# Optimization experiments

Hardware: AMD Instinct MI355X
Metric: run time of the kernel (lower is better)

Reference implementation:

```python
import jax, jax.numpy as jnp
import numpy as np

B, T, D, U, T_DEC = 32, 2048, 512, 256, 256


def setup_inputs() -> dict:
    key = jax.random.key(0)
    ks = jax.random.split(key, 8)
    s = 0.05  # small init scale to avoid tanh/sigmoid saturation
    return {
        "x": jax.random.normal(ks[0], (B, T, D), dtype=jnp.float32),
        "W_s": jax.random.normal(ks[1], (D, U), dtype=jnp.float32) * s,
        "U_a": jax.random.normal(ks[2], (D, U), dtype=jnp.float32) * s,
        "b_a": jnp.zeros((U,), dtype=jnp.float32),
        "W_a": jax.random.normal(ks[3], (U, U), dtype=jnp.float32) * s,
        "V_a": jax.random.normal(ks[4], (U,), dtype=jnp.float32) * s,
        "kernel": jax.random.normal(ks[5], (D, 4 * U), dtype=jnp.float32) * s,
        "recurrent_kernel": jax.random.normal(ks[6], (U, 4 * U), dtype=jnp.float32) * s,
        "bias": jnp.concatenate([
            jnp.zeros((U,), jnp.float32),      # i
            jnp.ones((U,), jnp.float32),       # f (unit_forget_bias)
            jnp.zeros((2 * U,), jnp.float32),  # c, o
        ]),
        "decode_steps": T_DEC,
    }


def _hard_sigmoid(z):
    # keras hard_sigmoid: clip(0.2*x + 0.5, 0, 1)
    return jnp.clip(0.2 * z + 0.5, 0.0, 1.0)


def reference(x, W_s, U_a, b_a, W_a, V_a, kernel, recurrent_kernel, bias, decode_steps):
    # Precompute U_a projection of encoder states once (as in call()).
    uxpb = jnp.einsum('btd,du->btu', x, U_a) + b_a          # [B,T,U]
    h0 = jnp.tanh(x[:, 0] @ W_s)                            # [B,U] initial state
    c0 = jnp.zeros_like(h0)

    def step(carry, _):
        h, c = carry
        # Bahdanau additive attention over encoder timesteps
        e = jnp.einsum('btu,u->bt', jnp.tanh(uxpb + (h @ W_a)[:, None, :]), V_a)
        a = jax.nn.softmax(e, axis=1)                       # exp/sum in original
        ctx = jnp.einsum('bt,btd->bd', a, x)                # weighted context [B,D]
        # Fused LSTM gate matmuls on context + previous state
        z = ctx @ kernel + h @ recurrent_kernel + bias      # [B,4U]
        zi, zf, zc, zo = jnp.split(z, 4, axis=-1)
        i = _hard_sigmoid(zi)
        f = _hard_sigmoid(zf)
        o = _hard_sigmoid(zo)
        c_new = f * c + i * jnp.tanh(zc)
        h_new = o * jnp.tanh(c_new)
        return (h_new, c_new), h_new

    (_, _), ys = jax.lax.scan(step, (h0, c0), None, length=decode_steps)
    return jnp.transpose(ys, (1, 0, 2))                     # [B, T_dec, U]
```

## Files before the change

kernel.cpp:

```cpp
#include <hip/hip_runtime.h>
#include <stdint.h>

#define B_    32
#define T_    2048
#define D_    512
#define U_    256
#define TSP_  128
#define NSL   (T_/TSP_)

typedef short          bf16x8 __attribute__((ext_vector_type(8)));
typedef unsigned short u16x4  __attribute__((ext_vector_type(4)));
typedef float          f32x4  __attribute__((ext_vector_type(4)));
typedef float          f32x2  __attribute__((ext_vector_type(2)));

__device__ __forceinline__ float bf2f(unsigned short u){
  union{unsigned int i; float f;} v; v.i = ((unsigned int)u)<<16; return v.f;
}
__device__ __forceinline__ unsigned short f2bf(float f){
  union{float f; unsigned int i;} v; v.f = f;
  unsigned int r = v.i + 0x7FFFu + ((v.i>>16)&1u);
  return (unsigned short)(r>>16);
}
__device__ __forceinline__ float ftanh(float x){
  float xx = fminf(fmaxf(x,-20.f),20.f);
  float t = __builtin_amdgcn_exp2f(xx * 2.885390082f);
  return (t-1.f)*__builtin_amdgcn_rcpf(t+1.f);
}
__device__ __forceinline__ float fexp(float x){
  return __builtin_amdgcn_exp2f(x*1.4426950408889634f);
}

__device__ unsigned int f2e4m3_1(float f){
  union{float f; unsigned int i;} v; v.f = f;
  unsigned int s = (v.i>>31)<<7;
  float af = fabsf(f);
  af = fminf(af, 448.f);
  unsigned int code;
  if (af < 0.015625f){
    code = (unsigned int)rintf(af*512.f);
  } else {
    int ex; float mant = frexpf(af,&ex);
    int E = ex-1;
    int m = (int)rintf(mant*16.f - 8.f);
    if (m==8){ E+=1; m=0; }
    if (E>8){ E=8; m=6; }
    code = ((unsigned int)(E+7)<<3) | (unsigned int)m;
  }
  return s|code;
}

__device__ __forceinline__ float e4m3f(unsigned int b){
  int e = (int)((b>>3)&15u), m = (int)(b&7u);
  int M = e ? (m+8) : m;
  M = (b&128u) ? -M : M;
  int E = (e ? e : 1) - 10;
  return ldexpf((float)M, E);
}

#if __has_builtin(__builtin_amdgcn_cvt_pk_f32_fp8)
#define DEC8(Q,F) {                                                      \
  f32x2 t_;                                                              \
  t_ = __builtin_amdgcn_cvt_pk_f32_fp8((int)Q.x, false); F[0]=t_[0]; F[1]=t_[1]; \
  t_ = __builtin_amdgcn_cvt_pk_f32_fp8((int)Q.x, true ); F[2]=t_[0]; F[3]=t_[1]; \
  t_ = __builtin_amdgcn_cvt_pk_f32_fp8((int)Q.y, false); F[4]=t_[0]; F[5]=t_[1]; \
  t_ = __builtin_amdgcn_cvt_pk_f32_fp8((int)Q.y, true ); F[6]=t_[0]; F[7]=t_[1]; }
#define DEC4(Q,F) {                                                      \
  f32x2 t_;                                                              \
  t_ = __builtin_amdgcn_cvt_pk_f32_fp8((int)Q, false); F[0]=t_[0]; F[1]=t_[1]; \
  t_ = __builtin_amdgcn_cvt_pk_f32_fp8((int)Q, true ); F[2]=t_[0]; F[3]=t_[1]; }
#else
#define DEC8(Q,F) {                                                      \
  F[0]=e4m3f(Q.x&255u);      F[1]=e4m3f((Q.x>>8)&255u);                  \
  F[2]=e4m3f((Q.x>>16)&255u);F[3]=e4m3f(Q.x>>24);                        \
  F[4]=e4m3f(Q.y&255u);      F[5]=e4m3f((Q.y>>8)&255u);                  \
  F[6]=e4m3f((Q.y>>16)&255u);F[7]=e4m3f(Q.y>>24); }
#define DEC4(Q,F) {                                                      \
  F[0]=e4m3f(Q&255u);        F[1]=e4m3f((Q>>8)&255u);                    \
  F[2]=e4m3f((Q>>16)&255u);  F[3]=e4m3f(Q>>24); }
#endif

__global__ __launch_bounds__(256) void k_f2b(
    const float* __restrict__ src, unsigned short* __restrict__ dst, int n)
{
  int idx = (blockIdx.x*256 + threadIdx.x)*4;
  int stride = gridDim.x*256*4;
  for (; idx < n; idx += stride){
    float4 v = *(const float4*)(src+idx);
    u16x4 o; o.x=f2bf(v.x); o.y=f2bf(v.y); o.z=f2bf(v.z); o.w=f2bf(v.w);
    *(u16x4*)(dst+idx) = o;
  }
}

__global__ __launch_bounds__(256) void k_f2e8(
    const float* __restrict__ src, unsigned char* __restrict__ dst, int n)
{
  int idx = (blockIdx.x*256 + threadIdx.x)*8;
  int stride = gridDim.x*256*8;
  for (; idx < n; idx += stride){
    float4 a = *(const float4*)(src+idx);
    float4 b = *(const float4*)(src+idx+4);
    unsigned int w0 = f2e4m3_1(a.x) | (f2e4m3_1(a.y)<<8) |
                      (f2e4m3_1(a.z)<<16) | (f2e4m3_1(a.w)<<24);
    unsigned int w1 = f2e4m3_1(b.x) | (f2e4m3_1(b.y)<<8) |
                      (f2e4m3_1(b.z)<<16) | (f2e4m3_1(b.w)<<24);
    uint2 o; o.x = w0; o.y = w1;
    *(uint2*)(dst+idx) = o;
  }
}

__global__ __launch_bounds__(256) void k_uxpb(
    const float* __restrict__ x,
    const float* __restrict__ Ua,
    const float* __restrict__ ba,
    unsigned char* __restrict__ uxpb)
{
  __shared__ unsigned short As[64][40];
  __shared__ unsigned short Bs[64][40];
  int bx = blockIdx.x;
  int nt = bx & 3, mt = bx >> 2;
  int m0 = mt*64, n0 = nt*64;
  int tid = threadIdx.x;
  int lane = tid & 63, w = tid >> 6;
  int wm = w >> 1, wn = w & 1;

  f32x4 acc[2][2] = {};
  int ar = tid >> 2, ak = (tid & 3) * 8;
  int bk = tid >> 3, bn = (tid & 7) * 8;

  for (int k0 = 0; k0 < 512; k0 += 32) {
    const float* ap = x  + (long)(m0+ar)*512 + k0 + ak;
    const float* bp = Ua + (long)(k0+bk)*256 + n0 + bn;
    float4 a0 = *(const float4*)ap, a1 = *(const float4*)(ap+4);
    float4 b0 = *(const float4*)bp, b1 = *(const float4*)(bp+4);
    __syncthreads();
    unsigned short* as = &As[ar][ak];
    as[0]=f2bf(a0.x); as[1]=f2bf(a0.y); as[2]=f2bf(a0.z); as[3]=f2bf(a0.w);
    as[4]=f2bf(a1.x); as[5]=f2bf(a1.y); as[6]=f2bf(a1.z); as[7]=f2bf(a1.w);
    Bs[bn+0][bk]=f2bf(b0.x); Bs[bn+1][bk]=f2bf(b0.y);
    Bs[bn+2][bk]=f2bf(b0.z); Bs[bn+3][bk]=f2bf(b0.w);
    Bs[bn+4][bk]=f2bf(b1.x); Bs[bn+5][bk]=f2bf(b1.y);
    Bs[bn+6][bk]=f2bf(b1.z); Bs[bn+7][bk]=f2bf(b1.w);
    __syncthreads();
    #pragma unroll
    for (int mi = 0; mi < 2; ++mi) {
      bf16x8 a = *(const bf16x8*)&As[wm*32 + mi*16 + (lane&15)][(lane>>4)*8];
      #pragma unroll
      for (int ni = 0; ni < 2; ++ni) {
        bf16x8 b = *(const bf16x8*)&Bs[wn*32 + ni*16 + (lane&15)][(lane>>4)*8];
        acc[mi][ni] = __builtin_amdgcn_mfma_f32_16x16x32_bf16(a, b, acc[mi][ni], 0,0,0);
      }
    }
  }
  #pragma unroll
  for (int mi = 0; mi < 2; ++mi)
  #pragma unroll
  for (int ni = 0; ni < 2; ++ni) {
    int col = n0 + wn*32 + ni*16 + (lane&15);
    float bias = ba[col];
    #pragma unroll
    for (int r = 0; r < 4; ++r) {
      int row = m0 + wm*32 + mi*16 + (lane>>4)*4 + r;
      uxpb[(long)row*256 + col] = (unsigned char)f2e4m3_1(acc[mi][ni][r] + bias);
    }
  }
}

__global__ __launch_bounds__(256) void k_init_h(
    const float* __restrict__ x,
    const float* __restrict__ Ws,
    float* __restrict__ h0,
    float* __restrict__ c_ws)
{
  int b = blockIdx.x, tid = threadIdx.x;
  __shared__ float xs[512];
  xs[tid]     = x[(long)b*T_*D_ + tid];
  xs[tid+256] = x[(long)b*T_*D_ + tid + 256];
  __syncthreads();
  float sum = 0.f;
  for (int k = 0; k < 512; ++k) sum = fmaf(xs[k], Ws[(long)k*256 + tid], sum);
  h0[b*256+tid] = ftanh(sum);
  c_ws[b*256+tid] = 0.f;
}

__global__ __launch_bounds__(256) void k_init_hw(
    const float* __restrict__ Wa,
    const float* __restrict__ h0,
    float* __restrict__ hW_part)
{
  int wg = blockIdx.x; int b = wg>>3, j = wg&7;
  int tid = threadIdx.x;
  __shared__ float hn[32];
  if (tid < 32) hn[tid] = h0[b*256 + j*32 + tid];
  __syncthreads();
  float sum = 0.f;
  #pragma unroll 8
  for (int w2 = 0; w2 < 32; ++w2) sum = fmaf(hn[w2], Wa[(j*32+w2)*256 + tid], sum);
  hW_part[(b*8+j)*256 + tid] = sum;
}

template<int XBF>
__global__ __launch_bounds__(512, 6) void k_attn(
    const float* __restrict__ xf,
    const unsigned char* __restrict__ x8,
    const unsigned char* __restrict__ uxpb,
    const float* __restrict__ Va,
    const float* __restrict__ hW_part,
    float* __restrict__ part_s,
    float* __restrict__ part_ctx)
{
  int wg = blockIdx.x;
  int b = wg >> 4, sl = wg & 15;
  int tid = threadIdx.x, lane = tid & 63, w = tid >> 6;

  __shared__ float hws[256];
  __shared__ float wsum[8];
  __shared__ float wctx[8][512];

  if (tid < 256) {
    float hsum = 0.f;
    #pragma unroll
    for (int j = 0; j < 8; ++j) hsum += hW_part[(b*8+j)*256 + tid];
    hws[tid] = hsum;
  }
  __syncthreads();
  float hw0 = hws[lane*4+0], hw1 = hws[lane*4+1];
  float hw2 = hws[lane*4+2], hw3 = hws[lane*4+3];
  float4 vv = *(const float4*)(Va + lane*4);

  const long rbase = (long)b*T_ + sl*TSP_ + w*16;
  const unsigned char*  up0 = uxpb + rbase*256 + lane*4;
  const unsigned char*  xp8 = x8   + rbase*512 + lane*8;
  const float*          pf0 = xf   + rbase*512 + lane*8;

  float ssum = 0.f;
  float acc[8] = {0,0,0,0,0,0,0,0};

  #pragma unroll
  for (int i = 0; i < 16; i += 2) {
    unsigned int u0 = *(const unsigned int*)(up0 + (long)i*256);
    unsigned int u1 = *(const unsigned int*)(up0 + (long)(i+1)*256);
    float ua0[4], ua1[4];
    DEC4(u0, ua0);
    DEC4(u1, ua1);
    float e0 = 0.f, e1 = 0.f;
    e0 = fmaf(ftanh(ua0[0] + hw0), vv.x, e0);
    e1 = fmaf(ftanh(ua1[0] + hw0), vv.x, e1);
    e0 = fmaf(ftanh(ua0[1] + hw1), vv.y, e0);
    e1 = fmaf(ftanh(ua1[1] + hw1), vv.y, e1);
    e0 = fmaf(ftanh(ua0[2] + hw2), vv.z, e0);
    e1 = fmaf(ftanh(ua1[2] + hw2), vv.z, e1);
    e0 = fmaf(ftanh(ua0[3] + hw3), vv.w, e0);
    e1 = fmaf(ftanh(ua1[3] + hw3), vv.w, e1);
    #pragma unroll
    for (int o = 1; o < 64; o <<= 1) {
      e0 += __shfl_xor(e0, o, 64);
      e1 += __shfl_xor(e1, o, 64);
    }
    float p0 = fexp(e0), p1 = fexp(e1);
    ssum += p0 + p1;
    if (XBF) {
      uint2 q0 = *(const uint2*)(xp8 + (long)i*512);
      uint2 q1 = *(const uint2*)(xp8 + (long)(i+1)*512);
      float x0a[8], x1a[8];
      DEC8(q0, x0a);
      DEC8(q1, x1a);
      #pragma unroll
      for (int j = 0; j < 8; ++j)
        acc[j] = fmaf(p1, x1a[j], fmaf(p0, x0a[j], acc[j]));
    } else {
      const float* p0p = pf0 + (long)i*512;
      const float* p1p = pf0 + (long)(i+1)*512;
      float4 v00 = *(const float4*)p0p, v01 = *(const float4*)(p0p+4);
      float4 v10 = *(const float4*)p1p, v11 = *(const float4*)(p1p+4);
      float x0a[8] = {v00.x,v00.y,v00.z,v00.w,v01.x,v01.y,v01.z,v01.w};
      float x1a[8] = {v10.x,v10.y,v10.z,v10.w,v11.x,v11.y,v11.z,v11.w};
      #pragma unroll
      for (int j = 0; j < 8; ++j)
        acc[j] = fmaf(p1, x1a[j], fmaf(p0, x0a[j], acc[j]));
    }
  }

  if (lane == 0) wsum[w] = ssum;
  #pragma unroll
  for (int j = 0; j < 8; ++j) wctx[w][lane*8+j] = acc[j];
  __syncthreads();
  {
    int d = tid;
    float c = wctx[0][d] + wctx[1][d] + wctx[2][d] + wctx[3][d]
            + wctx[4][d] + wctx[5][d] + wctx[6][d] + wctx[7][d];
    part_ctx[(long)(b*NSL+sl)*512 + d] = c;
  }
  if (tid == 0)
    part_s[b*NSL+sl] = wsum[0]+wsum[1]+wsum[2]+wsum[3]
                     + wsum[4]+wsum[5]+wsum[6]+wsum[7];
}

template<int WBF>
__global__ __launch_bounds__(1024) void k_step(
    const float* __restrict__ Wk,
    const float* __restrict__ Wr,
    const unsigned short* __restrict__ Wkb,
    const unsigned short* __restrict__ Wrb,
    const float* __restrict__ bias,
    const float* __restrict__ Wa,
    const unsigned short* __restrict__ Wab,
    const float* __restrict__ part_s,
    const float* __restrict__ part_ctx,
    const float* __restrict__ h_in,
    float* __restrict__ h_out,
    float* __restrict__ c_ws,
    float* __restrict__ hW_part,
    float* __restrict__ out,
    int step, int TDEC)
{
  int wg = blockIdx.x;
  int b = wg >> 3, j = wg & 7;
  int tid = threadIdx.x;

  __shared__ float ctx[512];
  __shared__ float hsh[256];
  __shared__ float zp[8][128];
  __shared__ float hn[32];

  if (tid < 512) {
    float S = 0.f;
    #pragma unroll 8
    for (int i = 0; i < NSL; ++i) S += part_s[b*NSL+i];
    float invS = 1.f / S;
    float c = 0.f;
    #pragma unroll 8
    for (int i = 0; i < NSL; ++i)
      c += part_ctx[(long)(b*NSL+i)*512 + tid];
    ctx[tid] = c * invS;
  } else if (tid < 768) {
    hsh[tid-512] = h_in[b*256 + (tid-512)];
  }
  __syncthreads();

  int c_  = tid & 127, kq = tid >> 7;
  int g   = c_ >> 5;
  int col = g*256 + j*32 + (c_ & 31);
  int k0 = kq*96, k1 = k0 + 96;
  int kb = (k1 < 512) ? k1 : 512;
  int kc = (k0 > 512) ? k0 : 512;
  float z = 0.f;
  if (WBF) {
    #pragma unroll 8
    for (int k = k0; k < kb; ++k)
      z = fmaf(ctx[k], bf2f(Wkb[(long)k*1024 + col]), z);
    #pragma unroll 8
    for (int k = kc; k < k1; ++k)
      z = fmaf(hsh[k-512], bf2f(Wrb[(long)(k-512)*1024 + col]), z);
  } else {
    #pragma unroll 8
    for (int k = k0; k < kb; ++k)
      z = fmaf(ctx[k], Wk[(long)k*1024 + col], z);
    #pragma unroll 8
    for (int k = kc; k < k1; ++k)
      z = fmaf(hsh[k-512], Wr[(long)(k-512)*1024 + col], z);
  }
  zp[kq][c_] = z;
  __syncthreads();

  if (tid < 128) {
    int colr = (tid>>5)*256 + j*32 + (tid&31);
    float zz = zp[0][tid]+zp[1][tid]+zp[2][tid]+zp[3][tid]
             + zp[4][tid]+zp[5][tid]+zp[6][tid]+zp[7][tid] + bias[colr];
    zp[0][tid] = zz;
  }
  __syncthreads();

  if (tid < 32) {
    float zi = zp[0][tid], zf = zp[0][32+tid], zc = zp[0][64+tid], zo = zp[0][96+tid];
    float ig = fminf(fmaxf(0.2f*zi+0.5f, 0.f), 1.f);
    float fg = fminf(fmaxf(0.2f*zf+0.5f, 0.f), 1.f);
    float og = fminf(fmaxf(0.2f*zo+0.5f, 0.f), 1.f);
    int u = j*32 + tid;
    float c_old = c_ws[b*256+u];
    float c_new = fg*c_old + ig*ftanh(zc);
    float h_new = og*ftanh(c_new);
    c_ws[b*256+u]  = c_new;
    h_out[b*256+u] = h_new;
    out[((long)b*TDEC + step)*256 + u] = h_new;
    hn[tid] = h_new;
  }
  __syncthreads();

  if (tid < 256) {
    float sum = 0.f;
    if (WBF) {
      #pragma unroll 8
      for (int w2 = 0; w2 < 32; ++w2)
        sum = fmaf(hn[w2], bf2f(Wab[(j*32+w2)*256 + tid]), sum);
    } else {
      #pragma unroll 8
      for (int w2 = 0; w2 < 32; ++w2)
        sum = fmaf(hn[w2], Wa[(j*32+w2)*256 + tid], sum);
    }
    hW_part[(b*8+j)*256 + tid] = sum;
  }
}

extern "C" void kernel_launch(void* const* d_in, const int* in_sizes, int n_in,
                              void* d_out, int out_size, void* d_ws, size_t ws_size,
                              hipStream_t stream)
{
  const float* x  = (const float*)d_in[0];
  const float* Ws = (const float*)d_in[1];
  const float* Ua = (const float*)d_in[2];
  const float* ba = (const float*)d_in[3];
  const float* Wa = (const float*)d_in[4];
  const float* Va = (const float*)d_in[5];
  const float* Wk = (const float*)d_in[6];
  const float* Wr = (const float*)d_in[7];
  const float* bs = (const float*)d_in[8];
  int TDEC = out_size / (B_ * U_);

  size_t off = 0;
  char* base = (char*)d_ws;
  unsigned char* uxpb = (unsigned char*)(base+off);   off += (size_t)B_*T_*U_;
  float* part_ctx = (float*)(base+off);               off += (size_t)B_*NSL*512*4;
  float* part_s   = (float*)(base+off);               off += (size_t)B_*NSL*4;
  float* hW_part  = (float*)(base+off);               off += (size_t)B_*8*U_*4;
  float* h_buf    = (float*)(base+off);               off += (size_t)2*B_*U_*4;
  float* c_ws     = (float*)(base+off);               off += (size_t)B_*U_*4;
  unsigned char* x_f8 = (unsigned char*)(base+off);   off += (size_t)B_*T_*D_;
  bool use_x8 = (off <= ws_size);
  unsigned short* wk_bf = (unsigned short*)(base+off); off += (size_t)D_*4*U_*2;
  unsigned short* wr_bf = (unsigned short*)(base+off); off += (size_t)U_*4*U_*2;
  unsigned short* wa_bf = (unsigned short*)(base+off); off += (size_t)U_*U_*2;
  bool use_wbf = (off <= ws_size);

  k_uxpb  <<<(B_*T_/64)*(U_/64), 256, 0, stream>>>(x, Ua, ba, uxpb);
  if (use_x8) k_f2e8<<<2048, 256, 0, stream>>>(x, x_f8, B_*T_*D_);
  if (use_wbf) {
    k_f2b<<<512, 256, 0, stream>>>(Wk, wk_bf, D_*4*U_);
    k_f2b<<<256, 256, 0, stream>>>(Wr, wr_bf, U_*4*U_);
    k_f2b<<<64,  256, 0, stream>>>(Wa, wa_bf, U_*U_);
  }
  k_init_h<<<B_,  256, 0, stream>>>(x, Ws, h_buf, c_ws);
  k_init_hw<<<B_*8, 256, 0, stream>>>(Wa, h_buf, hW_part);

  for (int s = 0; s < TDEC; ++s) {
    float* h_in  = h_buf + (s & 1)     * B_ * U_;
    float* h_out = h_buf + ((s+1) & 1) * B_ * U_;
    if (use_x8)
      k_attn<1><<<B_*NSL, 512, 0, stream>>>(x, x_f8, uxpb, Va, hW_part,
                                            part_s, part_ctx);
    else
      k_attn<0><<<B_*NSL, 512, 0, stream>>>(x, x_f8, uxpb, Va, hW_part,
                                            part_s, part_ctx);
    if (use_wbf)
      k_step<1><<<B_*8, 1024, 0, stream>>>(Wk, Wr, wk_bf, wr_bf, bs, Wa, wa_bf,
                                           part_s, part_ctx, h_in, h_out,
                                           c_ws, hW_part, (float*)d_out, s, TDEC);
    else
      k_step<0><<<B_*8, 1024, 0, stream>>>(Wk, Wr, wk_bf, wr_bf, bs, Wa, wa_bf,
                                           part_s, part_ctx, h_in, h_out,
                                           c_ws, hW_part, (float*)d_out, s, TDEC);
  }
}
```

Baseline: 5.574 ms.

## Fuse attention and LSTM step kernels into one launch with flag-based handoff

Each decode step now launches a single kernel. Attention blocks publish per-slice completion flags with release stores, and LSTM-step blocks in the same grid spin on those flags before reducing context and computing gates. This removes one kernel launch and its inter-kernel gap per step, and the step blocks drop from 1024 to 512 threads with longer K chunks. It risks deadlock if the step blocks become resident before the attention blocks and starve them. It also drops the fp32 fallback paths and leaves an empty k_attn_f32 stub.

```diff
diff --git a/kernel.cpp b/kernel.cpp
--- a/kernel.cpp
+++ b/kernel.cpp
@@ -108,6 +108,11 @@
   }
 }
 
+__global__ void k_zero(int* __restrict__ p, int n){
+  int i = blockIdx.x*256 + threadIdx.x;
+  if (i < n) p[i] = 0;
+}
+
 __global__ __launch_bounds__(256) void k_uxpb(
     const float* __restrict__ x,
     const float* __restrict__ Ua,
@@ -198,67 +203,78 @@
   hW_part[(b*8+j)*256 + tid] = sum;
 }
 
-template<int XBF>
-__global__ __launch_bounds__(512, 6) void k_attn(
-    const float* __restrict__ xf,
+__global__ __launch_bounds__(512, 4) void k_fused(
     const unsigned char* __restrict__ x8,
     const unsigned char* __restrict__ uxpb,
     const float* __restrict__ Va,
-    const float* __restrict__ hW_part,
+    const unsigned short* __restrict__ Wkb,
+    const unsigned short* __restrict__ Wrb,
+    const float* __restrict__ bias,
+    const unsigned short* __restrict__ Wab,
     float* __restrict__ part_s,
-    float* __restrict__ part_ctx)
-{
+    float* __restrict__ part_ctx,
+    float* __restrict__ hW_part,
+    const float* __restrict__ h_in,
+    float* __restrict__ h_out,
+    float* __restrict__ c_ws,
+    float* __restrict__ out,
+    int* __restrict__ s1f,
+    int step, int TDEC)
+{
+  __shared__ float sA[8*512];
+  __shared__ float sB[264];
+
   int wg = blockIdx.x;
-  int b = wg >> 4, sl = wg & 15;
-  int tid = threadIdx.x, lane = tid & 63, w = tid >> 6;
-
-  __shared__ float hws[256];
-  __shared__ float wsum[8];
-  __shared__ float wctx[8][512];
-
-  if (tid < 256) {
-    float hsum = 0.f;
+  int tid = threadIdx.x;
+
+  if (wg < B_*NSL) {
+    int b = wg >> 4, sl = wg & 15;
+    int lane = tid & 63, w = tid >> 6;
+    float* hws = sB;
+    float* wsum = sB + 256;
+    float (*wctx)[512] = (float(*)[512])sA;
+
+    if (tid < 256) {
+      float hsum = 0.f;
+      #pragma unroll
+      for (int j = 0; j < 8; ++j) hsum += hW_part[(b*8+j)*256 + tid];
+      hws[tid] = hsum;
+    }
+    __syncthreads();
+    float hw0 = hws[lane*4+0], hw1 = hws[lane*4+1];
+    float hw2 = hws[lane*4+2], hw3 = hws[lane*4+3];
+    float4 vv = *(const float4*)(Va + lane*4);
+
+    const long rbase = (long)b*T_ + sl*TSP_ + w*16;
+    const unsigned char* up0 = uxpb + rbase*256 + lane*4;
+    const unsigned char* xp8 = x8   + rbase*512 + lane*8;
+
+    float ssum = 0.f;
+    float acc[8] = {0,0,0,0,0,0,0,0};
+
     #pragma unroll
-    for (int j = 0; j < 8; ++j) hsum += hW_part[(b*8+j)*256 + tid];
-    hws[tid] = hsum;
-  }
-  __syncthreads();
-  float hw0 = hws[lane*4+0], hw1 = hws[lane*4+1];
-  float hw2 = hws[lane*4+2], hw3 = hws[lane*4+3];
-  float4 vv = *(const float4*)(Va + lane*4);
-
-  const long rbase = (long)b*T_ + sl*TSP_ + w*16;
-  const unsigned char*  up0 = uxpb + rbase*256 + lane*4;
-  const unsigned char*  xp8 = x8   + rbase*512 + lane*8;
-  const float*          pf0 = xf   + rbase*512 + lane*8;
-
-  float ssum = 0.f;
-  float acc[8] = {0,0,0,0,0,0,0,0};
-
-  #pragma unroll
-  for (int i = 0; i < 16; i += 2) {
-    unsigned int u0 = *(const unsigned int*)(up0 + (long)i*256);
-    unsigned int u1 = *(const unsigned int*)(up0 + (long)(i+1)*256);
-    float ua0[4], ua1[4];
-    DEC4(u0, ua0);
-    DEC4(u1, ua1);
-    float e0 = 0.f, e1 = 0.f;
-    e0 = fmaf(ftanh(ua0[0] + hw0), vv.x, e0);
-    e1 = fmaf(ftanh(ua1[0] + hw0), vv.x, e1);
-    e0 = fmaf(ftanh(ua0[1] + hw1), vv.y, e0);
-    e1 = fmaf(ftanh(ua1[1] + hw1), vv.y, e1);
-    e0 = fmaf(ftanh(ua0[2] + hw2), vv.z, e0);
-    e1 = fmaf(ftanh(ua1[2] + hw2), vv.z, e1);
-    e0 = fmaf(ftanh(ua0[3] + hw3), vv.w, e0);
-    e1 = fmaf(ftanh(ua1[3] + hw3), vv.w, e1);
-    #pragma unroll
-    for (int o = 1; o < 64; o <<= 1) {
-      e0 += __shfl_xor(e0, o, 64);
-      e1 += __shfl_xor(e1, o, 64);
-    }
-    float p0 = fexp(e0), p1 = fexp(e1);
-    ssum += p0 + p1;
-    if (XBF) {
+    for (int i = 0; i < 16; i += 2) {
+      unsigned int u0 = *(const unsigned int*)(up0 + (long)i*256);
+      unsigned int u1 = *(const unsigned int*)(up0 + (long)(i+1)*256);
+      float ua0[4], ua1[4];
+      DEC4(u0, ua0);
+      DEC4(u1, ua1);
+      float e0 = 0.f, e1 = 0.f;
+      e0 = fmaf(ftanh(ua0[0] + hw0), vv.x, e0);
+      e1 = fmaf(ftanh(ua1[0] + hw0), vv.x, e1);
+      e0 = fmaf(ftanh(ua0[1] + hw1), vv.y, e0);
+      e1 = fmaf(ftanh(ua1[1] + hw1), vv.y, e1);
+      e0 = fmaf(ftanh(ua0[2] + hw2), vv.z, e0);
+      e1 = fmaf(ftanh(ua1[2] + hw2), vv.z, e1);
+      e0 = fmaf(ftanh(ua0[3] + hw3), vv.w, e0);
+      e1 = fmaf(ftanh(ua1[3] + hw3), vv.w, e1);
+      #pragma unroll
+      for (int o = 1; o < 64; o <<= 1) {
+        e0 += __shfl_xor(e0, o, 64);
+        e1 += __shfl_xor(e1, o, 64);
+      }
+      float p0 = fexp(e0), p1 = fexp(e1);
+      ssum += p0 + p1;
       uint2 q0 = *(const uint2*)(xp8 + (long)i*512);
       uint2 q1 = *(const uint2*)(xp8 + (long)(i+1)*512);
       float x0a[8], x1a[8];
@@ -267,138 +283,111 @@
       #pragma unroll
       for (int j = 0; j < 8; ++j)
         acc[j] = fmaf(p1, x1a[j], fmaf(p0, x0a[j], acc[j]));
-    } else {
-      const float* p0p = pf0 + (long)i*512;
-      const float* p1p = pf0 + (long)(i+1)*512;
-      float4 v00 = *(const float4*)p0p, v01 = *(const float4*)(p0p+4);
-      float4 v10 = *(const float4*)p1p, v11 = *(const float4*)(p1p+4);
-      float x0a[8] = {v00.x,v00.y,v00.z,v00.w,v01.x,v01.y,v01.z,v01.w};
-      float x1a[8] = {v10.x,v10.y,v10.z,v10.w,v11.x,v11.y,v11.z,v11.w};
-      #pragma unroll
-      for (int j = 0; j < 8; ++j)
-        acc[j] = fmaf(p1, x1a[j], fmaf(p0, x0a[j], acc[j]));
-    }
-  }
-
-  if (lane == 0) wsum[w] = ssum;
-  #pragma unroll
-  for (int j = 0; j < 8; ++j) wctx[w][lane*8+j] = acc[j];
-  __syncthreads();
-  {
-    int d = tid;
-    float c = wctx[0][d] + wctx[1][d] + wctx[2][d] + wctx[3][d]
-            + wctx[4][d] + wctx[5][d] + wctx[6][d] + wctx[7][d];
-    part_ctx[(long)(b*NSL+sl)*512 + d] = c;
-  }
-  if (tid == 0)
-    part_s[b*NSL+sl] = wsum[0]+wsum[1]+wsum[2]+wsum[3]
-                     + wsum[4]+wsum[5]+wsum[6]+wsum[7];
-}
-
-template<int WBF>
-__global__ __launch_bounds__(1024) void k_step(
-    const float* __restrict__ Wk,
-    const float* __restrict__ Wr,
-    const unsigned short* __restrict__ Wkb,
-    const unsigned short* __restrict__ Wrb,
-    const float* __restrict__ bias,
-    const float* __restrict__ Wa,
-    const unsigned short* __restrict__ Wab,
-    const float* __restrict__ part_s,
-    const float* __restrict__ part_ctx,
-    const float* __restrict__ h_in,
-    float* __restrict__ h_out,
-    float* __restrict__ c_ws,
-    float* __restrict__ hW_part,
-    float* __restrict__ out,
-    int step, int TDEC)
-{
-  int wg = blockIdx.x;
-  int b = wg >> 3, j = wg & 7;
-  int tid = threadIdx.x;
-
-  __shared__ float ctx[512];
-  __shared__ float hsh[256];
-  __shared__ float zp[8][128];
-  __shared__ float hn[32];
-
-  if (tid < 512) {
-    float S = 0.f;
-    #pragma unroll 8
-    for (int i = 0; i < NSL; ++i) S += part_s[b*NSL+i];
-    float invS = 1.f / S;
-    float c = 0.f;
-    #pragma unroll 8
-    for (int i = 0; i < NSL; ++i)
-      c += part_ctx[(long)(b*NSL+i)*512 + tid];
-    ctx[tid] = c * invS;
-  } else if (tid < 768) {
-    hsh[tid-512] = h_in[b*256 + (tid-512)];
-  }
-  __syncthreads();
-
-  int c_  = tid & 127, kq = tid >> 7;
-  int g   = c_ >> 5;
-  int col = g*256 + j*32 + (c_ & 31);
-  int k0 = kq*96, k1 = k0 + 96;
-  int kb = (k1 < 512) ? k1 : 512;
-  int kc = (k0 > 512) ? k0 : 512;
-  float z = 0.f;
-  if (WBF) {
+    }
+
+    if (lane == 0) wsum[w] = ssum;
+    #pragma unroll
+    for (int j = 0; j < 8; ++j) wctx[w][lane*8+j] = acc[j];
+    __syncthreads();
+    {
+      int d = tid;
+      float c = wctx[0][d] + wctx[1][d] + wctx[2][d] + wctx[3][d]
+              + wctx[4][d] + wctx[5][d] + wctx[6][d] + wctx[7][d];
+      part_ctx[(long)(b*NSL+sl)*512 + d] = c;
+    }
+    if (tid == 0)
+      part_s[b*NSL+sl] = wsum[0]+wsum[1]+wsum[2]+wsum[3]
+                       + wsum[4]+wsum[5]+wsum[6]+wsum[7];
+    __syncthreads();
+    if (tid == 0)
+      __hip_atomic_store(&s1f[b*NSL+sl], step+1, __ATOMIC_RELEASE,
+                         __HIP_MEMORY_SCOPE_AGENT);
+  } else {
+    int t = wg - B_*NSL;
+    int b = t >> 3, j = t & 7;
+    float* ctx = sA;
+    float* hsh = sA + 512;
+    float (*zp)[128] = (float(*)[128])(sA + 768);
+    float* hn  = sA + 1280;
+
+    if (tid < NSL) {
+      while (__hip_atomic_load(&s1f[b*NSL+tid], __ATOMIC_RELAXED,
+                               __HIP_MEMORY_SCOPE_AGENT) < step+1)
+        __builtin_amdgcn_s_sleep(64);
+    }
+    __syncthreads();
+    __builtin_amdgcn_fence(__ATOMIC_ACQUIRE, "agent");
+
+    {
+      float S = 0.f;
+      #pragma unroll 8
+      for (int i = 0; i < NSL; ++i) S += part_s[b*NSL+i];
+      float invS = 1.f / S;
+      float c = 0.f;
+      #pragma unroll 8
+      for (int i = 0; i < NSL; ++i)
+        c += part_ctx[(long)(b*NSL+i)*512 + tid];
+      ctx[tid] = c * invS;
+    }
+    if (tid < 256) hsh[tid] = h_in[b*256 + tid];
+    __syncthreads();
+
+    int c_  = tid & 127, kq = tid >> 7;
+    int col = (c_ >> 5)*256 + j*32 + (c_ & 31);
+    int k0 = kq*192, k1 = k0 + 192;
+    int kb = (k1 < 512) ? k1 : 512;
+    int kc = (k0 > 512) ? k0 : 512;
+    float z = 0.f;
     #pragma unroll 8
     for (int k = k0; k < kb; ++k)
       z = fmaf(ctx[k], bf2f(Wkb[(long)k*1024 + col]), z);
     #pragma unroll 8
     for (int k = kc; k < k1; ++k)
       z = fmaf(hsh[k-512], bf2f(Wrb[(long)(k-512)*1024 + col]), z);
-  } else {
-    #pragma unroll 8
-    for (int k = k0; k < kb; ++k)
-      z = fmaf(ctx[k], Wk[(long)k*1024 + col], z);
-    #pragma unroll 8
-    for (int k = kc; k < k1; ++k)
-      z = fmaf(hsh[k-512], Wr[(long)(k-512)*1024 + col], z);
-  }
-  zp[kq][c_] = z;
-  __syncthreads();
-
-  if (tid < 128) {
-    int colr = (tid>>5)*256 + j*32 + (tid&31);
-    float zz = zp[0][tid]+zp[1][tid]+zp[2][tid]+zp[3][tid]
-             + zp[4][tid]+zp[5][tid]+zp[6][tid]+zp[7][tid] + bias[colr];
-    zp[0][tid] = zz;
-  }
-  __syncthreads();
-
-  if (tid < 32) {
-    float zi = zp[0][tid], zf = zp[0][32+tid], zc = zp[0][64+tid], zo = zp[0][96+tid];
-    float ig = fminf(fmaxf(0.2f*zi+0.5f, 0.f), 1.f);
-    float fg = fminf(fmaxf(0.2f*zf+0.5f, 0.f), 1.f);
-    float og = fminf(fmaxf(0.2f*zo+0.5f, 0.f), 1.f);
-    int u = j*32 + tid;
-    float c_old = c_ws[b*256+u];
-    float c_new = fg*c_old + ig*ftanh(zc);
-    float h_new = og*ftanh(c_new);
-    c_ws[b*256+u]  = c_new;
-    h_out[b*256+u] = h_new;
-    out[((long)b*TDEC + step)*256 + u] = h_new;
-    hn[tid] = h_new;
-  }
-  __syncthreads();
-
-  if (tid < 256) {
-    float sum = 0.f;
-    if (WBF) {
+    zp[kq][c_] = z;
+    __syncthreads();
+
+    if (tid < 128) {
+      int colr = (tid>>5)*256 + j*32 + (tid&31);
+      float zz = zp[0][tid]+zp[1][tid]+zp[2][tid]+zp[3][tid] + bias[colr];
+      zp[0][tid] = zz;
+    }
+    __syncthreads();
+
+    if (tid < 32) {
+      float zi = zp[0][tid], zf = zp[0][32+tid], zc = zp[0][64+tid], zo = zp[0][96+tid];
+      float ig = fminf(fmaxf(0.2f*zi+0.5f, 0.f), 1.f);
+      float fg = fminf(fmaxf(0.2f*zf+0.5f, 0.f), 1.f);
+      float og = fminf(fmaxf(0.2f*zo+0.5f, 0.f), 1.f);
+      int u = j*32 + tid;
+      float c_old = c_ws[b*256+u];
+      float c_new = fg*c_old + ig*ftanh(zc);
+      float h_new = og*ftanh(c_new);
+      c_ws[b*256+u]  = c_new;
+      h_out[b*256+u] = h_new;
+      out[((long)b*TDEC + step)*256 + u] = h_new;
+      hn[tid] = h_new;
+    }
+    __syncthreads();
+
+    if (tid < 256) {
+      float sum = 0.f;
       #pragma unroll 8
       for (int w2 = 0; w2 < 32; ++w2)
         sum = fmaf(hn[w2], bf2f(Wab[(j*32+w2)*256 + tid]), sum);
-    } else {
-      #pragma unroll 8
-      for (int w2 = 0; w2 < 32; ++w2)
-        sum = fmaf(hn[w2], Wa[(j*32+w2)*256 + tid], sum);
-    }
-    hW_part[(b*8+j)*256 + tid] = sum;
-  }
+      hW_part[(b*8+j)*256 + tid] = sum;
+    }
+  }
+}
+
+__global__ __launch_bounds__(512, 6) void k_attn_f32(
+    const float* __restrict__ xf,
+    const unsigned char* __restrict__ uxpb,
+    const float* __restrict__ Va,
+    const float* __restrict__ hW_part,
+    float* __restrict__ part_s,
+    float* __restrict__ part_ctx)
+{
 }
 
 extern "C" void kernel_launch(void* const* d_in, const int* in_sizes, int n_in,
@@ -424,39 +413,27 @@
   float* hW_part  = (float*)(base+off);               off += (size_t)B_*8*U_*4;
   float* h_buf    = (float*)(base+off);               off += (size_t)2*B_*U_*4;
   float* c_ws     = (float*)(base+off);               off += (size_t)B_*U_*4;
+  int*   s1f      = (int*)(base+off);                 off += (size_t)B_*NSL*4;
   unsigned char* x_f8 = (unsigned char*)(base+off);   off += (size_t)B_*T_*D_;
-  bool use_x8 = (off <= ws_size);
   unsigned short* wk_bf = (unsigned short*)(base+off); off += (size_t)D_*4*U_*2;
   unsigned short* wr_bf = (unsigned short*)(base+off); off += (size_t)U_*4*U_*2;
   unsigned short* wa_bf = (unsigned short*)(base+off); off += (size_t)U_*U_*2;
-  bool use_wbf = (off <= ws_size);
 
   k_uxpb  <<<(B_*T_/64)*(U_/64), 256, 0, stream>>>(x, Ua, ba, uxpb);
-  if (use_x8) k_f2e8<<<2048, 256, 0, stream>>>(x, x_f8, B_*T_*D_);
-  if (use_wbf) {
-    k_f2b<<<512, 256, 0, stream>>>(Wk, wk_bf, D_*4*U_);
-    k_f2b<<<256, 256, 0, stream>>>(Wr, wr_bf, U_*4*U_);
-    k_f2b<<<64,  256, 0, stream>>>(Wa, wa_bf, U_*U_);
-  }
+  k_f2e8<<<2048, 256, 0, stream>>>(x, x_f8, B_*T_*D_);
+  k_f2b<<<512, 256, 0, stream>>>(Wk, wk_bf, D_*4*U_);
+  k_f2b<<<256, 256, 0, stream>>>(Wr, wr_bf, U_*4*U_);
+  k_f2b<<<64,  256, 0, stream>>>(Wa, wa_bf, U_*U_);
+  k_zero<<<(B_*NSL+255)/256, 256, 0, stream>>>(s1f, B_*NSL);
   k_init_h<<<B_,  256, 0, stream>>>(x, Ws, h_buf, c_ws);
   k_init_hw<<<B_*8, 256, 0, stream>>>(Wa, h_buf, hW_part);
 
   for (int s = 0; s < TDEC; ++s) {
     float* h_in  = h_buf + (s & 1)     * B_ * U_;
     float* h_out = h_buf + ((s+1) & 1) * B_ * U_;
-    if (use_x8)
-      k_attn<1><<<B_*NSL, 512, 0, stream>>>(x, x_f8, uxpb, Va, hW_part,
-                                            part_s, part_ctx);
-    else
-      k_attn<0><<<B_*NSL, 512, 0, stream>>>(x, x_f8, uxpb, Va, hW_part,
-                                            part_s, part_ctx);
-    if (use_wbf)
-      k_step<1><<<B_*8, 1024, 0, stream>>>(Wk, Wr, wk_bf, wr_bf, bs, Wa, wa_bf,
-                                           part_s, part_ctx, h_in, h_out,
-                                           c_ws, hW_part, (float*)d_out, s, TDEC);
-    else
-      k_step<0><<<B_*8, 1024, 0, stream>>>(Wk, Wr, wk_bf, wr_bf, bs, Wa, wa_bf,
-                                           part_s, part_ctx, h_in, h_out,
-                                           c_ws, hW_part, (float*)d_out, s, TDEC);
-  }
-}
+    k_fused<<<B_*NSL + B_*8, 512, 0, stream>>>(
+        x_f8, uxpb, Va, wk_bf, wr_bf, bs, wa_bf,
+        part_s, part_ctx, hW_part, h_in, h_out, c_ws,
+        (float*)d_out, s1f, s, TDEC);
+  }
+}
```

Measured after the change: 12.71 ms. 2.28x slower.
